# Kernel optimization log

Measured on AMD Instinct MI355X. Metric: run time of the kernel, lower is better.

The kernel has to match this reference:

```python
import jax, jax.numpy as jnp
import numpy as np

B, T_IN = 128, 512
D_IN, ENC, HID, ATTN = 512, 512, 1024, 256
INPUT_SIZE = D_IN + ENC  # attention concatenates context onto the embedding


def setup_inputs() -> dict:
    key = jax.random.key(0)
    ks = jax.random.split(key, 16)
    s = lambda k, shape, fan: jax.random.normal(k, shape, jnp.float32) * (1.0 / np.sqrt(fan))
    return {
        "embed_decode": jax.random.normal(ks[0], (B, 1, D_IN), jnp.float32),
        "h0": jax.random.normal(ks[1], (1, B, HID), jnp.float32),
        "c0": jax.random.normal(ks[2], (1, B, HID), jnp.float32),
        "enc_output": jax.random.normal(ks[3], (B, T_IN, ENC), jnp.float32),
        # Luong attention params
        "W_ph": s(ks[4], (ATTN, HID), HID),      # project_hid
        "W_pe": s(ks[5], (ATTN, ENC), ENC),      # project_eo
        "w_fc2": s(ks[6], (ATTN,), ATTN),        # fc2 (out_dim 1)
        # LSTM params (PyTorch layout, gate order i,f,g,o)
        "W_ih": s(ks[7], (4 * HID, INPUT_SIZE), INPUT_SIZE),
        "W_hh": s(ks[8], (4 * HID, HID), HID),
        "b_ih": jnp.zeros((4 * HID,), jnp.float32),
        "b_hh": jnp.zeros((4 * HID,), jnp.float32),
        # linear_projection: (enc+hidden) -> hidden
        "W_proj": s(ks[9], (HID, ENC + HID), ENC + HID),
        "b_proj": jnp.zeros((HID,), jnp.float32),
        "enc_ctxt_mask": jnp.zeros((B, T_IN), jnp.bool_),  # True = padding
    }


def _decoder_step(embed_decode, h0, c0, enc_output, W_ph, W_pe, w_fc2,
                  W_ih, W_hh, b_ih, b_hh, W_proj, b_proj, enc_ctxt_mask):
    h_last = h0[-1]  # (B, HID) -- attention query (top-layer hidden)
    c_last = c0[-1]

    # Luong (additive) attention: tanh(Wq h + Wk e) . v
    ph = h_last @ W_ph.T                      # (B, ATTN)
    pe = jnp.einsum('bte,ae->bta', enc_output, W_pe)  # (B, T, ATTN)
    scores = jnp.tanh(ph[:, None, :] + pe) @ w_fc2    # (B, T)
    scores = jnp.where(enc_ctxt_mask, -jnp.inf, scores)
    aw = jax.nn.softmax(scores, axis=-1)               # (B, T)
    ctxt = jnp.einsum('bt,bte->be', aw, enc_output)    # (B, ENC)

    # single LSTM step on concatenated [embed, context]
    x = jnp.concatenate([embed_decode[:, 0, :], ctxt], axis=-1)  # (B, INPUT_SIZE)
    gates = x @ W_ih.T + b_ih + h_last @ W_hh.T + b_hh           # (B, 4*HID)
    i, f, g, o = jnp.split(gates, 4, axis=-1)
    c1 = jax.nn.sigmoid(f) * c_last + jax.nn.sigmoid(i) * jnp.tanh(g)
    h1 = jax.nn.sigmoid(o) * jnp.tanh(c1)

    # projection of [rnn_output, context]; dropout is identity in eval mode
    proj_in = jnp.concatenate([h1, ctxt], axis=-1)                # (B, ENC+HID)
    out = jnp.tanh(proj_in @ W_proj.T + b_proj)                   # (B, HID)
    return out[:, None, :], h1[None], c1[None]


def reference(embed_decode, h0, c0, enc_output, W_ph, W_pe, w_fc2,
              W_ih, W_hh, b_ih, b_hh, W_proj, b_proj, enc_ctxt_mask):
    return _decoder_step(embed_decode, h0, c0, enc_output, W_ph, W_pe, w_fc2,
                         W_ih, W_hh, b_ih, b_hh, W_proj, b_proj, enc_ctxt_mask)
```

## Files before the change

kernel.cpp:

```cpp
#include <hip/hip_runtime.h>
#include <cstddef>

typedef float  f32x4  __attribute__((ext_vector_type(4)));
typedef __bf16 bf16x8 __attribute__((ext_vector_type(8)));
typedef __bf16 bf16x4 __attribute__((ext_vector_type(4)));

#define DEV static __device__ __forceinline__

DEV float sigf(float x){ return 1.f/(1.f+__expf(-x)); }
DEV float tanh_f(float x){
  x = fminf(fmaxf(x, -20.f), 20.f);
  float e = __expf(2.f*x);
  return (e-1.f)/(e+1.f);
}

DEV bf16x8 cvt8(const float4 a, const float4 b){
  bf16x8 r;
  r[0]=(__bf16)a.x; r[1]=(__bf16)a.y; r[2]=(__bf16)a.z; r[3]=(__bf16)a.w;
  r[4]=(__bf16)b.x; r[5]=(__bf16)b.y; r[6]=(__bf16)b.z; r[7]=(__bf16)b.w;
  return r;
}

DEV void pin(bf16x8& v){
  f32x4 t = __builtin_bit_cast(f32x4, v);
  asm volatile("" : "+v"(t));
  v = __builtin_bit_cast(bf16x8, t);
}

__global__ void k_setup(const float* __restrict__ W_pe, __bf16* __restrict__ wpeX,
                        const float* __restrict__ h0, const float* __restrict__ W_ph,
                        float* __restrict__ ph, const float* __restrict__ embed,
                        float* __restrict__ xh)
{
  const int bid = blockIdx.x, tid = threadIdx.x;
  __shared__ float h_s[1024];
  if (bid < 64){
    const int idx = bid*256 + tid;
    const int l = idx & 63, sub = (idx >> 6) & 15, gt = idx >> 10;
    const float* p = W_pe + ((size_t)gt*16 + (l&15))*512 + sub*32 + (l>>4)*8;
    float4 v0 = *(const float4*)p;
    float4 v1 = *(const float4*)(p+4);
    *(bf16x8*)(wpeX + ((size_t)(gt*16 + sub)*64 + l)*8) = cvt8(v0, v1);
  } else if (bid < 192){
    const int b = bid - 64;
    for (int k = tid; k < 1024; k += 256) h_s[k] = h0[(size_t)b*1024 + k];
    __syncthreads();
    const float* wr = W_ph + (size_t)tid*1024;
    float acc = 0.f;
    for (int k = 0; k < 1024; k += 4){
      float4 w = *(const float4*)(wr + k);
      acc += w.x*h_s[k] + w.y*h_s[k+1] + w.z*h_s[k+2] + w.w*h_s[k+3];
    }
    ph[b*256 + tid] = acc;
  } else {
    const int b = bid - 192;
    *(float2*)(xh + (size_t)b*2048 + tid*2) = *(const float2*)(embed + (size_t)b*512 + tid*2);
    *(float4*)(xh + (size_t)b*2048 + 1024 + tid*4) = *(const float4*)(h0 + (size_t)b*1024 + tid*4);
  }
}

#define RMW 520
__global__ __launch_bounds__(512,1) void k_fused(
    const float* __restrict__ enc, const __bf16* __restrict__ wpeX,
    const float* __restrict__ ph, const float* __restrict__ w_fc2,
    const unsigned char* __restrict__ mask,
    float* __restrict__ partC, float* __restrict__ partL)
{
  const int th = blockIdx.x;
  const int b  = blockIdx.y;
  const int tid = threadIdx.x;
  const int w = tid >> 6, l = tid & 63;
  const int la = l & 15, g = l >> 4;

  __shared__ __align__(16) __bf16 rm[2][32*RMW];
  __shared__ float sred[8][32];
  __shared__ float p_s[32];
  __shared__ float ph_s[256], w2_s[256];

  if (tid < 256){ ph_s[tid] = ph[b*256 + tid]; w2_s[tid] = w_fc2[tid]; }

  bf16x8 Bf0[16], Bf1[16];
  {
    const __bf16* bp0 = wpeX + ((size_t)(w*2    )*16*64 + l)*8;
    const __bf16* bp1 = wpeX + ((size_t)(w*2 + 1)*16*64 + l)*8;
    #pragma unroll
    for (int kt = 0; kt < 16; ++kt){
      Bf0[kt] = *(const bf16x8*)(bp0 + (size_t)kt*512);
      Bf1[kt] = *(const bf16x8*)(bp1 + (size_t)kt*512);
    }
    #pragma unroll
    for (int kt = 0; kt < 16; ++kt){ pin(Bf0[kt]); pin(Bf1[kt]); }
  }

  const int t0 = th*256;
  const int srow = tid >> 7;
  const int scol = (tid & 127) * 4;
  const float* gsrc = enc + ((size_t)b*512 + t0 + srow)*512 + scol;

  float4 st[8];
  #pragma unroll
  for (int rr = 0; rr < 8; ++rr)
    st[rr] = *(const float4*)(gsrc + (size_t)rr*4*512);
  #pragma unroll
  for (int rr = 0; rr < 8; ++rr){
    float4 v = st[rr];
    bf16x4 bv; bv[0]=(__bf16)v.x; bv[1]=(__bf16)v.y; bv[2]=(__bf16)v.z; bv[3]=(__bf16)v.w;
    *(bf16x4*)&rm[0][(srow + rr*4)*RMW + scol] = bv;
  }
  __syncthreads();

  float cacc = 0.f;
  float Lacc = 0.f;

  for (int tile = 0; tile < 8; ++tile){
    const int cur = tile & 1;
    if (tile < 7){
      const float* gn = gsrc + (size_t)(tile+1)*32*512;
      #pragma unroll
      for (int rr = 0; rr < 8; ++rr)
        st[rr] = *(const float4*)(gn + (size_t)rr*4*512);
    }
    f32x4 acc00 = {0.f,0.f,0.f,0.f}, acc01 = acc00, acc10 = acc00, acc11 = acc00;
    const __bf16* rb = &rm[cur][0];
    #pragma unroll
    for (int kt = 0; kt < 16; ++kt){
      bf16x8 a0 = *(const bf16x8*)(rb + (la     )*RMW + kt*32 + g*8);
      bf16x8 a1 = *(const bf16x8*)(rb + (16 + la)*RMW + kt*32 + g*8);
      acc00 = __builtin_amdgcn_mfma_f32_16x16x32_bf16(a0, Bf0[kt], acc00, 0,0,0);
      acc01 = __builtin_amdgcn_mfma_f32_16x16x32_bf16(a0, Bf1[kt], acc01, 0,0,0);
      acc10 = __builtin_amdgcn_mfma_f32_16x16x32_bf16(a1, Bf0[kt], acc10, 0,0,0);
      acc11 = __builtin_amdgcn_mfma_f32_16x16x32_bf16(a1, Bf1[kt], acc11, 0,0,0);
    }
    {
      const float phv0 = ph_s[w*32 + la],      w2v0 = w2_s[w*32 + la];
      const float phv1 = ph_s[w*32 + 16 + la], w2v1 = w2_s[w*32 + 16 + la];
      #pragma unroll
      for (int gt = 0; gt < 2; ++gt){
        const f32x4 pa = gt ? acc10 : acc00;
        const f32x4 pb = gt ? acc11 : acc01;
        #pragma unroll
        for (int r = 0; r < 4; ++r){
          float s = tanh_f(pa[r] + phv0)*w2v0 + tanh_f(pb[r] + phv1)*w2v1;
          s += __shfl_xor(s, 1, 16);
          s += __shfl_xor(s, 2, 16);
          s += __shfl_xor(s, 4, 16);
          s += __shfl_xor(s, 8, 16);
          if (la == 0) sred[w][gt*16 + g*4 + r] = s;
        }
      }
    }
    if (tile < 7){
      #pragma unroll
      for (int rr = 0; rr < 8; ++rr){
        float4 v = st[rr];
        bf16x4 bv; bv[0]=(__bf16)v.x; bv[1]=(__bf16)v.y; bv[2]=(__bf16)v.z; bv[3]=(__bf16)v.w;
        *(bf16x4*)&rm[cur^1][(srow + rr*4)*RMW + scol] = bv;
      }
    }
    __syncthreads();
    if (tid < 32){
      const int t = tid;
      float s = sred[0][t]+sred[1][t]+sred[2][t]+sred[3][t]
              + sred[4][t]+sred[5][t]+sred[6][t]+sred[7][t];
      const bool mk = mask[b*512 + t0 + tile*32 + t] != 0;
      float p = mk ? 0.f : __expf(s);
      p_s[t] = p;
      Lacc += p;
    }
    __syncthreads();
    {
      float s0 = 0.f, s1 = 0.f, s2 = 0.f, s3 = 0.f;
      const __bf16* rp = &rm[cur][tid];
      #pragma unroll
      for (int t = 0; t < 32; t += 4){
        s0 += p_s[t  ] * (float)rp[(t  )*RMW];
        s1 += p_s[t+1] * (float)rp[(t+1)*RMW];
        s2 += p_s[t+2] * (float)rp[(t+2)*RMW];
        s3 += p_s[t+3] * (float)rp[(t+3)*RMW];
      }
      cacc += (s0+s1)+(s2+s3);
    }
    __syncthreads();
  }

  partC[((size_t)th*128 + b)*512 + tid] = cacc;
  if (tid < 32){
    float Ls = Lacc;
    Ls += __shfl_xor(Ls, 1, 32);
    Ls += __shfl_xor(Ls, 2, 32);
    Ls += __shfl_xor(Ls, 4, 32);
    Ls += __shfl_xor(Ls, 8, 32);
    Ls += __shfl_xor(Ls, 16, 32);
    if (tid == 0) partL[th*128 + b] = Ls;
  }
}

__global__ void k_comb(const float* __restrict__ partC, const float* __restrict__ partL,
                       float* __restrict__ xh, float* __restrict__ hc)
{
  const int b = blockIdx.x, e = threadIdx.x;
  float L = partL[b] + partL[128 + b];
  float v = (partC[(size_t)b*512 + e] + partC[(size_t)(128 + b)*512 + e]) / L;
  xh[(size_t)b*2048 + 512 + e] = v;
  hc[(size_t)b*1536 + 1024 + e] = v;
}

__global__ __launch_bounds__(256,2) void k_gemm_part(
    const float* __restrict__ A, int lda,
    const float* __restrict__ W1, int ldw1,
    const float* __restrict__ W2, int ldw2, int ksplit,
    float* __restrict__ Cpart, int ldc, int Kloc)
{
  const int jt = blockIdx.x * 32;
  const int kc = blockIdx.y;
  const int koff = kc * Kloc;
  const int tid = threadIdx.x;
  const int w = tid >> 6, lane = tid & 63;
  const int la = lane & 15, g = lane >> 4;

  __shared__ __align__(16) __bf16 A_s[128][40];
  __shared__ __align__(16) __bf16 B_s[32][40];

  f32x4 acc[2][2];
  #pragma unroll
  for (int i = 0; i < 2; ++i)
    #pragma unroll
    for (int j = 0; j < 2; ++j) acc[i][j] = (f32x4){0.f,0.f,0.f,0.f};

  const int ar = tid >> 1, ac = (tid & 1) * 16;
  const int br = tid >> 3, bc = (tid & 7) * 4;

  for (int kl = 0; kl < Kloc; kl += 32){
    const int kk = koff + kl;
    {
      const float* p = A + (size_t)ar*lda + kk + ac;
      float4 v0 = *(const float4*)(p);
      float4 v1 = *(const float4*)(p+4);
      float4 v2 = *(const float4*)(p+8);
      float4 v3 = *(const float4*)(p+12);
      *(bf16x8*)&A_s[ar][ac]   = cvt8(v0,v1);
      *(bf16x8*)&A_s[ar][ac+8] = cvt8(v2,v3);
    }
    {
      const float* wp = (kk < ksplit)
          ? (W1 + (size_t)(jt+br)*ldw1 + kk + bc)
          : (W2 + (size_t)(jt+br)*ldw2 + (kk - ksplit) + bc);
      float4 v = *(const float4*)wp;
      bf16x4 bv;
      bv[0]=(__bf16)v.x; bv[1]=(__bf16)v.y; bv[2]=(__bf16)v.z; bv[3]=(__bf16)v.w;
      *(bf16x4*)&B_s[br][bc] = bv;
    }
    __syncthreads();
    bf16x8 a0 = *(const bf16x8*)&A_s[w*32 + la][g*8];
    bf16x8 a1 = *(const bf16x8*)&A_s[w*32 + 16 + la][g*8];
    bf16x8 b0 = *(const bf16x8*)&B_s[la][g*8];
    bf16x8 b1 = *(const bf16x8*)&B_s[16 + la][g*8];
    acc[0][0] = __builtin_amdgcn_mfma_f32_16x16x32_bf16(a0, b0, acc[0][0], 0,0,0);
    acc[0][1] = __builtin_amdgcn_mfma_f32_16x16x32_bf16(a0, b1, acc[0][1], 0,0,0);
    acc[1][0] = __builtin_amdgcn_mfma_f32_16x16x32_bf16(a1, b0, acc[1][0], 0,0,0);
    acc[1][1] = __builtin_amdgcn_mfma_f32_16x16x32_bf16(a1, b1, acc[1][1], 0,0,0);
    __syncthreads();
  }

  float* cp = Cpart + (size_t)kc*128*ldc;
  #pragma unroll
  for (int mfi = 0; mfi < 2; ++mfi)
    #pragma unroll
    for (int nf = 0; nf < 2; ++nf)
      #pragma unroll
      for (int r = 0; r < 4; ++r){
        int m = w*32 + mfi*16 + g*4 + r;
        int j = jt + nf*16 + la;
        cp[(size_t)m*ldc + j] = acc[mfi][nf][r];
      }
}

__global__ void k_lstm_fin(const float* __restrict__ partG, const float* __restrict__ b_ih,
                           const float* __restrict__ b_hh, const float* __restrict__ c0,
                           float* __restrict__ out, float* __restrict__ hc)
{
  const int idx = blockIdx.x*256 + threadIdx.x;
  const int b = idx >> 10, h = idx & 1023;
  float gi = b_ih[h]        + b_hh[h];
  float gf = b_ih[1024 + h] + b_hh[1024 + h];
  float gg = b_ih[2048 + h] + b_hh[2048 + h];
  float go = b_ih[3072 + h] + b_hh[3072 + h];
  #pragma unroll
  for (int kc = 0; kc < 4; ++kc){
    const float* gp = partG + ((size_t)kc*128 + b)*4096;
    gi += gp[h]; gf += gp[1024 + h]; gg += gp[2048 + h]; go += gp[3072 + h];
  }
  float c1 = sigf(gf)*c0[idx] + sigf(gi)*tanh_f(gg);
  float h1 = sigf(go)*tanh_f(c1);
  out[131072 + idx] = h1;
  out[262144 + idx] = c1;
  hc[(size_t)b*1536 + h] = h1;
}

__global__ void k_proj_fin(const float* __restrict__ partP, const float* __restrict__ b_proj,
                           float* __restrict__ out)
{
  const int idx = blockIdx.x*256 + threadIdx.x;
  const int b = idx >> 10, j = idx & 1023;
  float s = b_proj[j];
  #pragma unroll
  for (int kc = 0; kc < 4; ++kc)
    s += partP[((size_t)kc*128 + b)*1024 + j];
  out[idx] = tanh_f(s);
}

extern "C" void kernel_launch(void* const* d_in, const int* in_sizes, int n_in,
                              void* d_out, int out_size, void* d_ws, size_t ws_size,
                              hipStream_t stream)
{
  const float* embed  = (const float*)d_in[0];
  const float* h0     = (const float*)d_in[1];
  const float* c0     = (const float*)d_in[2];
  const float* enc    = (const float*)d_in[3];
  const float* W_ph   = (const float*)d_in[4];
  const float* W_pe   = (const float*)d_in[5];
  const float* w_fc2  = (const float*)d_in[6];
  const float* W_ih   = (const float*)d_in[7];
  const float* W_hh   = (const float*)d_in[8];
  const float* b_ih   = (const float*)d_in[9];
  const float* b_hh   = (const float*)d_in[10];
  const float* W_proj = (const float*)d_in[11];
  const float* b_proj = (const float*)d_in[12];
  const unsigned char* mask = (const unsigned char*)d_in[13];

  float* ws     = (float*)d_ws;
  float* ph     = ws;
  float* xh     = ws + 32768;
  float* hc     = ws + 294912;
  float* partC  = ws + 491520;
  float* partL  = ws + 622592;
  float* partG  = ws + 622848;
  float* partP  = ws + 2720000;
  __bf16* wpeX  = (__bf16*)(ws + 3244288);
  float* out    = (float*)d_out;

  k_setup <<<320, 256, 0, stream>>>(W_pe, wpeX, h0, W_ph, ph, embed, xh);
  k_fused <<<dim3(2,128), 512, 0, stream>>>(enc, wpeX, ph, w_fc2, mask,
                                            partC, partL);
  k_comb  <<<128, 512, 0, stream>>>(partC, partL, xh, hc);
  k_gemm_part<<<dim3(128,4), 256, 0, stream>>>(xh, 2048, W_ih, 1024, W_hh, 1024, 1024,
                                               partG, 4096, 512);
  k_lstm_fin<<<512, 256, 0, stream>>>(partG, b_ih, b_hh, c0, out, hc);
  k_gemm_part<<<dim3(32,4), 256, 0, stream>>>(hc, 1536, W_proj, 1536, nullptr, 0, 1536,
                                              partP, 1024, 384);
  k_proj_fin<<<512, 256, 0, stream>>>(partP, b_proj, out);
}
```

Measured before the change: 108.0 us.

## Software-pipeline attention tiles with triple LDS buffer and two-deep prefetch

Restructures the per-block tile loop into a fully unrolled software pipeline. It uses three LDS buffers and two register staging sets, so global loads run two tiles ahead and the PV accumulation of one tile overlaps the QK MFMA of the next. This removes one barrier per tile. The mask is preloaded into shared memory once instead of read from global inside each softmax step. The cost is more LDS use (a third buffer) and more registers for the second staging set, which could spill or limit scheduling.

```diff
diff --git a/kernel.cpp b/kernel.cpp
--- a/kernel.cpp
+++ b/kernel.cpp
@@ -72,10 +72,11 @@
   const int w = tid >> 6, l = tid & 63;
   const int la = l & 15, g = l >> 4;
 
-  __shared__ __align__(16) __bf16 rm[2][32*RMW];
+  __shared__ __align__(16) __bf16 rm[3][32*RMW];
   __shared__ float sred[8][32];
   __shared__ float p_s[32];
   __shared__ float ph_s[256], w2_s[256];
+  __shared__ unsigned char mask_s[256];
 
   if (tid < 256){ ph_s[tid] = ph[b*256 + tid]; w2_s[tid] = w_fc2[tid]; }
 
@@ -97,91 +98,107 @@
   const int scol = (tid & 127) * 4;
   const float* gsrc = enc + ((size_t)b*512 + t0 + srow)*512 + scol;
 
-  float4 st[8];
-  #pragma unroll
-  for (int rr = 0; rr < 8; ++rr)
-    st[rr] = *(const float4*)(gsrc + (size_t)rr*4*512);
-  #pragma unroll
-  for (int rr = 0; rr < 8; ++rr){
-    float4 v = st[rr];
-    bf16x4 bv; bv[0]=(__bf16)v.x; bv[1]=(__bf16)v.y; bv[2]=(__bf16)v.z; bv[3]=(__bf16)v.w;
-    *(bf16x4*)&rm[0][(srow + rr*4)*RMW + scol] = bv;
-  }
-  __syncthreads();
-
+  float4 st0[8], st1[8];
   float cacc = 0.f;
   float Lacc = 0.f;
 
-  for (int tile = 0; tile < 8; ++tile){
-    const int cur = tile & 1;
-    if (tile < 7){
-      const float* gn = gsrc + (size_t)(tile+1)*32*512;
-      #pragma unroll
-      for (int rr = 0; rr < 8; ++rr)
-        st[rr] = *(const float4*)(gn + (size_t)rr*4*512);
-    }
-    f32x4 acc00 = {0.f,0.f,0.f,0.f}, acc01 = acc00, acc10 = acc00, acc11 = acc00;
-    const __bf16* rb = &rm[cur][0];
-    #pragma unroll
-    for (int kt = 0; kt < 16; ++kt){
-      bf16x8 a0 = *(const bf16x8*)(rb + (la     )*RMW + kt*32 + g*8);
-      bf16x8 a1 = *(const bf16x8*)(rb + (16 + la)*RMW + kt*32 + g*8);
-      acc00 = __builtin_amdgcn_mfma_f32_16x16x32_bf16(a0, Bf0[kt], acc00, 0,0,0);
-      acc01 = __builtin_amdgcn_mfma_f32_16x16x32_bf16(a0, Bf1[kt], acc01, 0,0,0);
-      acc10 = __builtin_amdgcn_mfma_f32_16x16x32_bf16(a1, Bf0[kt], acc10, 0,0,0);
-      acc11 = __builtin_amdgcn_mfma_f32_16x16x32_bf16(a1, Bf1[kt], acc11, 0,0,0);
-    }
-    {
-      const float phv0 = ph_s[w*32 + la],      w2v0 = w2_s[w*32 + la];
-      const float phv1 = ph_s[w*32 + 16 + la], w2v1 = w2_s[w*32 + 16 + la];
-      #pragma unroll
-      for (int gt = 0; gt < 2; ++gt){
-        const f32x4 pa = gt ? acc10 : acc00;
-        const f32x4 pb = gt ? acc11 : acc01;
-        #pragma unroll
-        for (int r = 0; r < 4; ++r){
-          float s = tanh_f(pa[r] + phv0)*w2v0 + tanh_f(pb[r] + phv1)*w2v1;
-          s += __shfl_xor(s, 1, 16);
-          s += __shfl_xor(s, 2, 16);
-          s += __shfl_xor(s, 4, 16);
-          s += __shfl_xor(s, 8, 16);
-          if (la == 0) sred[w][gt*16 + g*4 + r] = s;
-        }
-      }
-    }
-    if (tile < 7){
-      #pragma unroll
-      for (int rr = 0; rr < 8; ++rr){
-        float4 v = st[rr];
-        bf16x4 bv; bv[0]=(__bf16)v.x; bv[1]=(__bf16)v.y; bv[2]=(__bf16)v.z; bv[3]=(__bf16)v.w;
-        *(bf16x4*)&rm[cur^1][(srow + rr*4)*RMW + scol] = bv;
-      }
-    }
-    __syncthreads();
-    if (tid < 32){
-      const int t = tid;
-      float s = sred[0][t]+sred[1][t]+sred[2][t]+sred[3][t]
-              + sred[4][t]+sred[5][t]+sred[6][t]+sred[7][t];
-      const bool mk = mask[b*512 + t0 + tile*32 + t] != 0;
-      float p = mk ? 0.f : __expf(s);
-      p_s[t] = p;
-      Lacc += p;
-    }
-    __syncthreads();
-    {
-      float s0 = 0.f, s1 = 0.f, s2 = 0.f, s3 = 0.f;
-      const __bf16* rp = &rm[cur][tid];
-      #pragma unroll
-      for (int t = 0; t < 32; t += 4){
-        s0 += p_s[t  ] * (float)rp[(t  )*RMW];
-        s1 += p_s[t+1] * (float)rp[(t+1)*RMW];
-        s2 += p_s[t+2] * (float)rp[(t+2)*RMW];
-        s3 += p_s[t+3] * (float)rp[(t+3)*RMW];
-      }
-      cacc += (s0+s1)+(s2+s3);
-    }
-    __syncthreads();
-  }
+#define ISSUE(ST, TI) {                                                       \
+    const float* gn = gsrc + (size_t)(TI)*32*512;                             \
+    _Pragma("unroll")                                                         \
+    for (int rr = 0; rr < 8; ++rr)                                            \
+      ST[rr] = *(const float4*)(gn + (size_t)rr*4*512);                       \
+  }
+
+#define WRITE_RM(BUF, ST) {                                                   \
+    _Pragma("unroll")                                                         \
+    for (int rr = 0; rr < 8; ++rr){                                           \
+      float4 v = ST[rr];                                                      \
+      bf16x4 bv; bv[0]=(__bf16)v.x; bv[1]=(__bf16)v.y;                        \
+      bv[2]=(__bf16)v.z; bv[3]=(__bf16)v.w;                                   \
+      *(bf16x4*)&rm[BUF][(srow + rr*4)*RMW + scol] = bv;                      \
+    } }
+
+#define QK_EPI(BUF) {                                                         \
+    f32x4 acc00 = {0.f,0.f,0.f,0.f}, acc01 = acc00, acc10 = acc00, acc11 = acc00; \
+    const __bf16* rb = &rm[BUF][0];                                           \
+    _Pragma("unroll")                                                         \
+    for (int kt = 0; kt < 16; ++kt){                                          \
+      bf16x8 a0 = *(const bf16x8*)(rb + (la     )*RMW + kt*32 + g*8);         \
+      bf16x8 a1 = *(const bf16x8*)(rb + (16 + la)*RMW + kt*32 + g*8);         \
+      acc00 = __builtin_amdgcn_mfma_f32_16x16x32_bf16(a0, Bf0[kt], acc00, 0,0,0); \
+      acc01 = __builtin_amdgcn_mfma_f32_16x16x32_bf16(a0, Bf1[kt], acc01, 0,0,0); \
+      acc10 = __builtin_amdgcn_mfma_f32_16x16x32_bf16(a1, Bf0[kt], acc10, 0,0,0); \
+      acc11 = __builtin_amdgcn_mfma_f32_16x16x32_bf16(a1, Bf1[kt], acc11, 0,0,0); \
+    }                                                                         \
+    const float phv0 = ph_s[w*32 + la],      w2v0 = w2_s[w*32 + la];          \
+    const float phv1 = ph_s[w*32 + 16 + la], w2v1 = w2_s[w*32 + 16 + la];     \
+    _Pragma("unroll")                                                         \
+    for (int gt = 0; gt < 2; ++gt){                                           \
+      const f32x4 pa = gt ? acc10 : acc00;                                    \
+      const f32x4 pb = gt ? acc11 : acc01;                                    \
+      _Pragma("unroll")                                                       \
+      for (int r = 0; r < 4; ++r){                                            \
+        float s = tanh_f(pa[r] + phv0)*w2v0 + tanh_f(pb[r] + phv1)*w2v1;      \
+        s += __shfl_xor(s, 1, 16);                                            \
+        s += __shfl_xor(s, 2, 16);                                            \
+        s += __shfl_xor(s, 4, 16);                                            \
+        s += __shfl_xor(s, 8, 16);                                            \
+        if (la == 0) sred[w][gt*16 + g*4 + r] = s;                            \
+      }                                                                       \
+    } }
+
+#define PV(BUF) {                                                             \
+    float s0 = 0.f, s1 = 0.f, s2 = 0.f, s3 = 0.f;                             \
+    const __bf16* rp = &rm[BUF][tid];                                         \
+    _Pragma("unroll")                                                         \
+    for (int t = 0; t < 32; t += 4){                                          \
+      s0 += p_s[t  ] * (float)rp[(t  )*RMW];                                  \
+      s1 += p_s[t+1] * (float)rp[(t+1)*RMW];                                  \
+      s2 += p_s[t+2] * (float)rp[(t+2)*RMW];                                  \
+      s3 += p_s[t+3] * (float)rp[(t+3)*RMW];                                  \
+    }                                                                         \
+    cacc += (s0+s1)+(s2+s3);                                                  \
+  }
+
+#define SM(TILE)                                                              \
+  if (tid < 32){                                                              \
+    const int t = tid;                                                        \
+    float s = sred[0][t]+sred[1][t]+sred[2][t]+sred[3][t]                     \
+            + sred[4][t]+sred[5][t]+sred[6][t]+sred[7][t];                    \
+    float p = mask_s[(TILE)*32 + t] ? 0.f : __expf(s);                        \
+    p_s[t] = p;                                                               \
+    Lacc += p;                                                                \
+  }
+
+  ISSUE(st0, 0)
+  WRITE_RM(0, st0)
+  ISSUE(st1, 1)
+  if (tid < 256) mask_s[tid] = mask[b*512 + t0 + tid];
+  __syncthreads();
+
+  ISSUE(st0, 2)  QK_EPI(0)  WRITE_RM(1, st1)
+  __syncthreads();  SM(0)  __syncthreads();
+  ISSUE(st1, 3)  PV(0)  QK_EPI(1)  WRITE_RM(2, st0)
+  __syncthreads();  SM(1)  __syncthreads();
+  ISSUE(st0, 4)  PV(1)  QK_EPI(2)  WRITE_RM(0, st1)
+  __syncthreads();  SM(2)  __syncthreads();
+  ISSUE(st1, 5)  PV(2)  QK_EPI(0)  WRITE_RM(1, st0)
+  __syncthreads();  SM(3)  __syncthreads();
+  ISSUE(st0, 6)  PV(0)  QK_EPI(1)  WRITE_RM(2, st1)
+  __syncthreads();  SM(4)  __syncthreads();
+  ISSUE(st1, 7)  PV(1)  QK_EPI(2)  WRITE_RM(0, st0)
+  __syncthreads();  SM(5)  __syncthreads();
+  PV(2)  QK_EPI(0)  WRITE_RM(1, st1)
+  __syncthreads();  SM(6)  __syncthreads();
+  PV(0)  QK_EPI(1)
+  __syncthreads();  SM(7)  __syncthreads();
+  PV(1)
+
+#undef ISSUE
+#undef WRITE_RM
+#undef QK_EPI
+#undef PV
+#undef SM
 
   partC[((size_t)th*128 + b)*512 + tid] = cacc;
   if (tid < 32){
```

Result: slower. 223.2 us (+106.6%).

## Merge the two per-batch attention blocks into one 1024-thread block

Applied to the files above, without the earlier changes.

The attention kernel previously launched two 512-thread blocks per batch row, one per half of the time axis. They are now combined into a single 1024-thread block per batch row, with shared buffers indexed by half, so ph and w_fc2 are staged once and the grid becomes 128 blocks. This halves the block count, which on a device with 256 CUs may leave many CUs idle. Shared memory per block roughly doubles and register pressure under a 1024-thread launch bound may cause spills given the 32 pinned B fragments per thread. Block-wide syncs now couple the two halves.

```diff
diff --git a/kernel.cpp b/kernel.cpp
--- a/kernel.cpp
+++ b/kernel.cpp
@@ -60,24 +60,25 @@
 }
 
 #define RMW 520
-__global__ __launch_bounds__(512,1) void k_fused(
+__global__ __launch_bounds__(1024,1) void k_fused(
     const float* __restrict__ enc, const __bf16* __restrict__ wpeX,
     const float* __restrict__ ph, const float* __restrict__ w_fc2,
     const unsigned char* __restrict__ mask,
     float* __restrict__ partC, float* __restrict__ partL)
 {
-  const int th = blockIdx.x;
-  const int b  = blockIdx.y;
-  const int tid = threadIdx.x;
+  const int b   = blockIdx.x;
+  const int gtid = threadIdx.x;
+  const int th  = gtid >> 9;
+  const int tid = gtid & 511;
   const int w = tid >> 6, l = tid & 63;
   const int la = l & 15, g = l >> 4;
 
-  __shared__ __align__(16) __bf16 rm[2][32*RMW];
-  __shared__ float sred[8][32];
-  __shared__ float p_s[32];
+  __shared__ __align__(16) __bf16 rm[2][2][32*RMW];
+  __shared__ float sred[2][8][32];
+  __shared__ float p_s[2][32];
   __shared__ float ph_s[256], w2_s[256];
 
-  if (tid < 256){ ph_s[tid] = ph[b*256 + tid]; w2_s[tid] = w_fc2[tid]; }
+  if (gtid < 256){ ph_s[gtid] = ph[b*256 + gtid]; w2_s[gtid] = w_fc2[gtid]; }
 
   bf16x8 Bf0[16], Bf1[16];
   {
@@ -105,7 +106,7 @@
   for (int rr = 0; rr < 8; ++rr){
     float4 v = st[rr];
     bf16x4 bv; bv[0]=(__bf16)v.x; bv[1]=(__bf16)v.y; bv[2]=(__bf16)v.z; bv[3]=(__bf16)v.w;
-    *(bf16x4*)&rm[0][(srow + rr*4)*RMW + scol] = bv;
+    *(bf16x4*)&rm[th][0][(srow + rr*4)*RMW + scol] = bv;
   }
   __syncthreads();
 
@@ -121,7 +122,7 @@
         st[rr] = *(const float4*)(gn + (size_t)rr*4*512);
     }
     f32x4 acc00 = {0.f,0.f,0.f,0.f}, acc01 = acc00, acc10 = acc00, acc11 = acc00;
-    const __bf16* rb = &rm[cur][0];
+    const __bf16* rb = &rm[th][cur][0];
     #pragma unroll
     for (int kt = 0; kt < 16; ++kt){
       bf16x8 a0 = *(const bf16x8*)(rb + (la     )*RMW + kt*32 + g*8);
@@ -145,7 +146,7 @@
           s += __shfl_xor(s, 2, 16);
           s += __shfl_xor(s, 4, 16);
           s += __shfl_xor(s, 8, 16);
-          if (la == 0) sred[w][gt*16 + g*4 + r] = s;
+          if (la == 0) sred[th][w][gt*16 + g*4 + r] = s;
         }
       }
     }
@@ -154,29 +155,30 @@
       for (int rr = 0; rr < 8; ++rr){
         float4 v = st[rr];
         bf16x4 bv; bv[0]=(__bf16)v.x; bv[1]=(__bf16)v.y; bv[2]=(__bf16)v.z; bv[3]=(__bf16)v.w;
-        *(bf16x4*)&rm[cur^1][(srow + rr*4)*RMW + scol] = bv;
+        *(bf16x4*)&rm[th][cur^1][(srow + rr*4)*RMW + scol] = bv;
       }
     }
     __syncthreads();
     if (tid < 32){
       const int t = tid;
-      float s = sred[0][t]+sred[1][t]+sred[2][t]+sred[3][t]
-              + sred[4][t]+sred[5][t]+sred[6][t]+sred[7][t];
+      float s = sred[th][0][t]+sred[th][1][t]+sred[th][2][t]+sred[th][3][t]
+              + sred[th][4][t]+sred[th][5][t]+sred[th][6][t]+sred[th][7][t];
       const bool mk = mask[b*512 + t0 + tile*32 + t] != 0;
       float p = mk ? 0.f : __expf(s);
-      p_s[t] = p;
+      p_s[th][t] = p;
       Lacc += p;
     }
     __syncthreads();
     {
       float s0 = 0.f, s1 = 0.f, s2 = 0.f, s3 = 0.f;
-      const __bf16* rp = &rm[cur][tid];
+      const __bf16* rp = &rm[th][cur][tid];
+      const float* pp = p_s[th];
       #pragma unroll
       for (int t = 0; t < 32; t += 4){
-        s0 += p_s[t  ] * (float)rp[(t  )*RMW];
-        s1 += p_s[t+1] * (float)rp[(t+1)*RMW];
-        s2 += p_s[t+2] * (float)rp[(t+2)*RMW];
-        s3 += p_s[t+3] * (float)rp[(t+3)*RMW];
+        s0 += pp[t  ] * (float)rp[(t  )*RMW];
+        s1 += pp[t+1] * (float)rp[(t+1)*RMW];
+        s2 += pp[t+2] * (float)rp[(t+2)*RMW];
+        s3 += pp[t+3] * (float)rp[(t+3)*RMW];
       }
       cacc += (s0+s1)+(s2+s3);
     }
@@ -340,8 +342,7 @@
   float* out    = (float*)d_out;
 
   k_setup <<<320, 256, 0, stream>>>(W_pe, wpeX, h0, W_ph, ph, embed, xh);
-  k_fused <<<dim3(2,128), 512, 0, stream>>>(enc, wpeX, ph, w_fc2, mask,
-                                            partC, partL);
+  k_fused <<<128, 1024, 0, stream>>>(enc, wpeX, ph, w_fc2, mask, partC, partL);
   k_comb  <<<128, 512, 0, stream>>>(partC, partL, xh, hc);
   k_gemm_part<<<dim3(128,4), 256, 0, stream>>>(xh, 2048, W_ih, 1024, W_hh, 1024, 1024,
                                                partG, 4096, 512);
```

After: 228.5 us. +111.5%, slower.
